# Performance work log

Measured on AMD Instinct MI355X. Metric: run time of the kernel, lower is better.

Reference implementation:

```python
import jax, jax.numpy as jnp
import numpy as np

E = 384      # EMBEDDING_SIZE
DFF = 1536
H = 6        # NUM_HEADS
D = E // H   # ATTN_DIM_SIZE = 64
T = 256      # SEQ_LEN
L = 6        # NUM_BLOCKS
V = 65       # VOCAB_SIZE
NPOS = 10000.0
B = 128


def _pos_encoding():
    i = jnp.arange(T, dtype=jnp.float32)[:, None]
    k = jnp.arange(E // 2, dtype=jnp.float32)[None, :]
    ang = i / jnp.power(NPOS, 2.0 * k / E)   # [T, E/2]
    pe = jnp.zeros((T, E), dtype=jnp.float32)
    pe = pe.at[:, 0::2].set(jnp.sin(ang))
    pe = pe.at[:, 1::2].set(jnp.cos(ang))
    return pe


def setup_inputs() -> dict:
    key = jax.random.key(0)
    ks = jax.random.split(key, 24)
    s = 0.02
    n = lambda k, shp: (jax.random.normal(k, shp, dtype=jnp.float32) * s)
    inp = {
        'tokens': jax.random.randint(ks[0], (B, T), 0, V),
        'pos_enc': _pos_encoding(),
        'emb': n(ks[1], (V, E)),
        # stacked per-layer params [L, ...]; weights stored as (in, out)
        'Wq': n(ks[2], (L, E, E)), 'bq': jnp.zeros((L, E)),
        'Wk': n(ks[3], (L, E, E)), 'bk': jnp.zeros((L, E)),
        'Wv': n(ks[4], (L, E, E)), 'bv': jnp.zeros((L, E)),
        'Wo': n(ks[5], (L, E, E)), 'bo': jnp.zeros((L, E)),
        'ln1_g': jnp.ones((L, E)), 'ln1_b': jnp.zeros((L, E)),
        'W1': n(ks[6], (L, E, DFF)), 'c1': jnp.zeros((L, DFF)),
        'W2': n(ks[7], (L, DFF, E)), 'c2': jnp.zeros((L, E)),
        'ln2_g': jnp.ones((L, E)), 'ln2_b': jnp.zeros((L, E)),
        'Wl': n(ks[8], (E, V)), 'bl': jnp.zeros((V,)),
    }
    return inp


def _layer_norm(x, g, b, eps=1e-5):
    mu = jnp.mean(x, axis=-1, keepdims=True)
    var = jnp.mean((x - mu) ** 2, axis=-1, keepdims=True)
    return (x - mu) * jax.lax.rsqrt(var + eps) * g + b


def _decoder(tokens, pos_enc, emb, Wq, bq, Wk, bk, Wv, bv, Wo, bo,
             ln1_g, ln1_b, W1, c1, W2, c2, ln2_g, ln2_b, Wl, bl):
    b_, t_ = tokens.shape
    x = emb[tokens] + pos_enc[None, :t_, :]            # [B,T,E]
    causal = jnp.tril(jnp.ones((t_, t_), dtype=bool)) # tril mask
    scale = D ** (-0.5)

    def block(x, p):
        (wq, bq_, wk, bk_, wv, bv_, wo, bo_, g1, be1, w1, c1_, w2, c2_, g2, be2) = p
        h = _layer_norm(x, g1, be1)
        q = (h @ wq + bq_).reshape(b_, t_, H, D)
        k = (h @ wk + bk_).reshape(b_, t_, H, D)
        v = (h @ wv + bv_).reshape(b_, t_, H, D)
        scores = jnp.einsum('bqhd,bkhd->bhqk', q, k) * scale
        scores = jnp.where(causal[None, None], scores, -jnp.inf)
        attn = jax.nn.softmax(scores, axis=-1)
        o = jnp.einsum('bhqk,bkhd->bqhd', attn, v).reshape(b_, t_, E)
        x = x + (o @ wo + bo_)
        h2 = _layer_norm(x, g2, be2)
        x = x + (jax.nn.relu(h2 @ w1 + c1_) @ w2 + c2_)
        return x, None

    params = (Wq, bq, Wk, bk, Wv, bv, Wo, bo, ln1_g, ln1_b, W1, c1, W2, c2, ln2_g, ln2_b)
    x, _ = jax.lax.scan(block, x, params)
    return x @ Wl + bl                                 # [B,T,V]


def reference(tokens, pos_enc, emb, Wq, bq, Wk, bk, Wv, bv, Wo, bo,
              ln1_g, ln1_b, W1, c1, W2, c2, ln2_g, ln2_b, Wl, bl):
    return _decoder(tokens, pos_enc, emb, Wq, bq, Wk, bk, Wv, bv, Wo, bo,
                    ln1_g, ln1_b, W1, c1, W2, c2, ln2_g, ln2_b, Wl, bl)
```

## Files before the change

### kernel.cpp

```cpp
#include <hip/hip_runtime.h>
#include <hip/hip_bf16.h>
#include <stdint.h>

constexpr int E   = 384;
constexpr int DFF = 1536;
constexpr int NH  = 6;
constexpr int HD  = 64;
constexpr int T   = 256;
constexpr int NL  = 6;
constexpr int NV  = 65;
constexpr int BB  = 128;
constexpr int MTOT = BB * T;
constexpr int CB  = 32;

typedef __bf16 bf16;
typedef __attribute__((ext_vector_type(8))) __bf16 bf16x8;
typedef __attribute__((ext_vector_type(4))) __bf16 bf16x4;
typedef __attribute__((ext_vector_type(4))) float floatx4;

#define GBM 128
#define GBN 128
#define GBK 64

template <int MODE, int SWAP>
__device__ __forceinline__ void gemm_body(
    char* AsB,
    const bf16* __restrict__ A, int lda,
    const bf16* __restrict__ Bf,
    const float* __restrict__ bias,
    void* __restrict__ Cv, void* __restrict__ Cv2, int ldc,
    int nt, int mt, int Nvalid, int K, int relu)
{
    int tid = threadIdx.x;
    int lane = tid & 63;
    int wid = tid >> 6;
    int wm = wid >> 2, wn = wid & 3;
    int lq = lane >> 4, lr = lane & 15;

    const bf16* Ab = A + (long)mt * GBM * lda;

    int srow = tid >> 3;
    int skc  = (tid & 7) * 8;
    const bf16* Arow = Ab + (long)srow * lda + skc;
    const long a2 = 64 * (long)lda;

    int wcol = ((tid & 7) * 16) ^ ((srow & 7) << 4);
    char* wp0 = AsB + srow * 128 + wcol;

    int nk = K / GBK;
    int nks = K / 32;
    const bf16* Bq = Bf + ((long)(nt * 8 + wn * 2) * nks) * 512 + lane * 8;

    floatx4 zero = {0.f, 0.f, 0.f, 0.f};
    floatx4 acc[4][2];
#pragma unroll
    for (int i = 0; i < 4; i++)
#pragma unroll
        for (int j = 0; j < 2; j++) acc[i][j] = zero;

    const char* rp0 = AsB + (wm * 64 + lr) * 128;
    int rx0 = (lq * 16) ^ ((lr & 7) << 4);

    bf16x8 ra[2];
    ra[0] = *(const bf16x8*)(Arow);
    ra[1] = *(const bf16x8*)(Arow + a2);
    *(bf16x8*)(wp0)        = ra[0];
    *(bf16x8*)(wp0 + 8192) = ra[1];
    if (nk > 1) {
        ra[0] = *(const bf16x8*)(Arow + GBK);
        ra[1] = *(const bf16x8*)(Arow + a2 + GBK);
    }
    __syncthreads();

    for (int ki = 0; ki < nk; ki++) {
        int ib = ki & 1;
        bf16x8 bb[4];
#pragma unroll
        for (int ni = 0; ni < 2; ni++)
#pragma unroll
            for (int kh = 0; kh < 2; kh++)
                bb[ni * 2 + kh] =
                    *(const bf16x8*)(Bq + ((long)ni * nks + 2 * ki + kh) * 512);
        if (ki + 1 < nk) {
            char* wp = wp0 + (1 - ib) * 16384;
            *(bf16x8*)(wp)        = ra[0];
            *(bf16x8*)(wp + 8192) = ra[1];
        }
        if (ki + 2 < nk) {
            long koff = (long)(ki + 2) * GBK;
            ra[0] = *(const bf16x8*)(Arow + koff);
            ra[1] = *(const bf16x8*)(Arow + a2 + koff);
        }
        const char* rp = rp0 + ib * 16384;

        bf16x8 af[4];
#pragma unroll
        for (int mi = 0; mi < 4; mi++)
            af[mi] = *(const bf16x8*)(rp + mi * 2048 + rx0);
#pragma unroll
        for (int mi = 0; mi < 4; mi++)
#pragma unroll
            for (int ni = 0; ni < 2; ni++)
                acc[mi][ni] = SWAP
                    ? __builtin_amdgcn_mfma_f32_16x16x32_bf16(bb[ni * 2], af[mi], acc[mi][ni], 0, 0, 0)
                    : __builtin_amdgcn_mfma_f32_16x16x32_bf16(af[mi], bb[ni * 2], acc[mi][ni], 0, 0, 0);
#pragma unroll
        for (int mi = 0; mi < 4; mi++)
            af[mi] = *(const bf16x8*)(rp + mi * 2048 + (rx0 ^ 64));
#pragma unroll
        for (int mi = 0; mi < 4; mi++)
#pragma unroll
            for (int ni = 0; ni < 2; ni++)
                acc[mi][ni] = SWAP
                    ? __builtin_amdgcn_mfma_f32_16x16x32_bf16(bb[ni * 2 + 1], af[mi], acc[mi][ni], 0, 0, 0)
                    : __builtin_amdgcn_mfma_f32_16x16x32_bf16(af[mi], bb[ni * 2 + 1], acc[mi][ni], 0, 0, 0);
        __syncthreads();
    }

    int m0 = mt * GBM, n0 = nt * GBN;
#pragma unroll
    for (int mi = 0; mi < 4; mi++) {
#pragma unroll
        for (int ni = 0; ni < 2; ni++) {
            floatx4 v = acc[mi][ni];
            if (SWAP) {
                int rowL = m0 + wm * 64 + mi * 16 + lr;
                int col0 = n0 + wn * 32 + ni * 16 + lq * 4;
                if (MODE == 5) {
                    bf16x4 pv;
#pragma unroll
                    for (int r = 0; r < 4; r++) pv[r] = (bf16)(v[r] + bias[col0 + r]);
                    *(bf16x4*)((bf16*)Cv + (long)rowL * 768 + col0) = pv;
                } else if (MODE == 1) {
                    bf16* Cp = (bf16*)Cv;
                    bf16x4* ptr = (bf16x4*)(Cp + (long)rowL * ldc + col0);
                    bf16x4 old = *ptr;
                    bf16x4 pv;
#pragma unroll
                    for (int r = 0; r < 4; r++)
                        pv[r] = (bf16)((float)old[r] + v[r] + bias[col0 + r]);
                    *ptr = pv;
                } else if (MODE == 4) {
                    float* Cp = (float*)Cv;
#pragma unroll
                    for (int r = 0; r < 4; r++)
                        if (col0 + r < Nvalid)
                            Cp[(long)rowL * ldc + col0 + r] = v[r] + bias[col0 + r];
                } else {
                    if (col0 < Nvalid) {
                        bf16x4 pv;
#pragma unroll
                        for (int r = 0; r < 4; r++) {
                            float x = v[r] + (bias ? bias[col0 + r] : 0.f);
                            if (relu) x = fmaxf(x, 0.f);
                            pv[r] = (bf16)x;
                        }
                        *(bf16x4*)((bf16*)Cv + (long)rowL * ldc + col0) = pv;
                    }
                }
            } else {
                int row0 = m0 + wm * 64 + mi * 16 + lq * 4;
                int colL = n0 + wn * 32 + ni * 16 + lr;
                float bv = bias[colL];
                bf16x4 pv;
#pragma unroll
                for (int r = 0; r < 4; r++) pv[r] = (bf16)(v[r] + bv);
                int bidx = row0 >> 8, pos = row0 & 255, e = colL - 768;
                *(bf16x4*)((bf16*)Cv2 + (long)bidx * (E * T) + (long)e * T + pos) = pv;
            }
        }
    }
}

template <int MODE>
__global__ __launch_bounds__(512, 4) void k_gemm(
    const bf16* __restrict__ A, int lda,
    const bf16* __restrict__ Bf,
    const float* __restrict__ bias,
    void* __restrict__ Cv, void* __restrict__ Cv2, int ldc,
    int Mtiles, int Ntiles, int Nvalid, int K,
    int relu)
{
    __shared__ __align__(16) char AsB[2 * 16384];

    int nb = gridDim.x;
    int per = nb >> 3;
    int bphys = blockIdx.x;
    int bid = (bphys & 7) * per + (bphys >> 3);

    int nt = bid % Ntiles;
    int mt = bid / Ntiles;

    if (MODE == 5 && nt >= 6)
        gemm_body<5, 0>(AsB, A, lda, Bf, bias, Cv, Cv2, ldc, nt, mt, Nvalid, K, relu);
    else
        gemm_body<MODE, 1>(AsB, A, lda, Bf, bias, Cv, Cv2, ldc, nt, mt, Nvalid, K, relu);
}

__global__ __launch_bounds__(256) void k_attn(
    const bf16* __restrict__ qk, const bf16* __restrict__ vt,
    bf16* __restrict__ o)
{
    int nb = gridDim.x;
    int per = nb >> 3;
    int bphys = blockIdx.x;
    int bid = (bphys & 7) * per + (bphys >> 3);

    int qt = bid & 3; bid >>= 2;
    int h = bid % NH; int b = bid / NH;
    int tid = threadIdx.x;
    int lane = tid & 63;
    int w = tid >> 6;
    int lq = lane >> 4;
    int lr = lane & 15;

    __shared__ __align__(16) bf16 Ks[256 * 72];
    __shared__ __align__(16) bf16 Vs[64 * 264];

    const bf16* qbase = qk + (long)(b * T + qt * 64 + w * 16) * 768 + h * 64;
    const bf16* kbase = qk + (long)(b * T) * 768 + 384 + h * 64;
    const bf16* vbase = vt + ((long)b * E + h * 64) * T;

#pragma unroll
    for (int i = 0; i < 8; i++) {
        int idx = i * 256 + tid;
        int row = idx >> 3, off = (idx & 7) * 8;
        *(bf16x8*)(&Ks[row * 72 + off]) = *(const bf16x8*)(kbase + (long)row * 768 + off);
    }
#pragma unroll
    for (int i = 0; i < 8; i++) {
        int idx = i * 256 + tid;
        int row = idx >> 5, off = (idx & 31) * 8;
        *(bf16x8*)(&Vs[row * 264 + off]) = *(const bf16x8*)(vbase + (long)row * 256 + off);
    }

    bf16x8 aq0 = *(const bf16x8*)(qbase + (long)lr * 768 + lq * 8);
    bf16x8 aq1 = *(const bf16x8*)(qbase + (long)lr * 768 + 32 + lq * 8);

    __syncthreads();

    const int ntmax = qt * 4 + 3;
    floatx4 zero = {0.f, 0.f, 0.f, 0.f};
    floatx4 s[16];
#pragma unroll
    for (int nt = 0; nt < 16; nt++) s[nt] = zero;

#pragma unroll
    for (int nt = 0; nt < 16; nt++) {
        if (nt <= ntmax) {
            const bf16* kp = &Ks[(nt * 16 + lr) * 72 + lq * 8];
            bf16x8 b0 = *(const bf16x8*)(kp);
            bf16x8 b1 = *(const bf16x8*)(kp + 32);
            s[nt] = __builtin_amdgcn_mfma_f32_16x16x32_bf16(aq0, b0, s[nt], 0, 0, 0);
            s[nt] = __builtin_amdgcn_mfma_f32_16x16x32_bf16(aq1, b1, s[nt], 0, 0, 0);
        }
    }

    int trow0 = qt * 64 + w * 16 + lq * 4;
    float m4[4] = {-3e38f, -3e38f, -3e38f, -3e38f};
#pragma unroll
    for (int nt = 0; nt < 16; nt++) {
        if (nt <= ntmax) {
            int tc = nt * 16 + lr;
#pragma unroll
            for (int r = 0; r < 4; r++) {
                float v = s[nt][r] * 0.125f;
                if (tc > trow0 + r) v = -3e38f;
                s[nt][r] = v;
                m4[r] = fmaxf(m4[r], v);
            }
        }
    }
#pragma unroll
    for (int r = 0; r < 4; r++) {
#pragma unroll
        for (int off = 1; off < 16; off <<= 1)
            m4[r] = fmaxf(m4[r], __shfl_xor(m4[r], off, 64));
    }

    float l4[4] = {0.f, 0.f, 0.f, 0.f};
#pragma unroll
    for (int nt = 0; nt < 16; nt++) {
        if (nt <= ntmax) {
#pragma unroll
            for (int r = 0; r < 4; r++) {
                float pv = __expf(s[nt][r] - m4[r]);
                l4[r] += pv;
                s[nt][r] = pv;
            }
        }
    }
#pragma unroll
    for (int r = 0; r < 4; r++) {
#pragma unroll
        for (int off = 1; off < 16; off <<= 1)
            l4[r] += __shfl_xor(l4[r], off, 64);
    }

    __syncthreads();

    bf16* P = Ks + w * (16 * 264);
#pragma unroll
    for (int nt = 0; nt < 16; nt++) {
        if (nt <= ntmax) {
#pragma unroll
            for (int r = 0; r < 4; r++)
                P[(lq * 4 + r) * 264 + nt * 16 + lr] = (bf16)s[nt][r];
        }
    }

    floatx4 oacc[4];
#pragma unroll
    for (int nd = 0; nd < 4; nd++) oacc[nd] = zero;
    const int kkmax = 2 * (qt + 1);
#pragma unroll
    for (int kk = 0; kk < 8; kk++) {
        if (kk < kkmax) {
            bf16x8 ap = *(const bf16x8*)(&P[lr * 264 + kk * 32 + lq * 8]);
#pragma unroll
            for (int nd = 0; nd < 4; nd++) {
                bf16x8 bv = *(const bf16x8*)(&Vs[(nd * 16 + lr) * 264 + kk * 32 + lq * 8]);
                oacc[nd] = __builtin_amdgcn_mfma_f32_16x16x32_bf16(ap, bv, oacc[nd], 0, 0, 0);
            }
        }
    }

#pragma unroll
    for (int r = 0; r < 4; r++) {
        float inv = 1.0f / l4[r];
        long rowg = (long)b * T + trow0 + r;
#pragma unroll
        for (int nd = 0; nd < 4; nd++) {
            o[rowg * E + h * 64 + nd * 16 + lr] = (bf16)(oacc[nd][r] * inv);
        }
    }
}

__global__ void k_ln(const bf16* __restrict__ x, const float* __restrict__ g,
                     const float* __restrict__ b, bf16* __restrict__ h) {
    int row = blockIdx.x * 4 + (threadIdx.x >> 6);
    int lane = threadIdx.x & 63;
    const bf16* xr = x + (long)row * E;
    float v[6];
    float s = 0.f;
#pragma unroll
    for (int i = 0; i < 6; i++) { v[i] = (float)xr[lane + 64 * i]; s += v[i]; }
#pragma unroll
    for (int o = 1; o < 64; o <<= 1) s += __shfl_xor(s, o, 64);
    float mu = s * (1.0f / E);
    float q = 0.f;
#pragma unroll
    for (int i = 0; i < 6; i++) { float d = v[i] - mu; q += d * d; }
#pragma unroll
    for (int o = 1; o < 64; o <<= 1) q += __shfl_xor(q, o, 64);
    float rs = rsqrtf(q * (1.0f / E) + 1e-5f);
    bf16* hr = h + (long)row * E;
#pragma unroll
    for (int i = 0; i < 6; i++) {
        int c = lane + 64 * i;
        hr[c] = (bf16)((v[i] - mu) * rs * g[c] + b[c]);
    }
}

__global__ void k_transpose_frag(const float* __restrict__ W, bf16* __restrict__ Wf,
                                 int K, int N, int NPAD) {
    long idx = (long)blockIdx.x * 256 + threadIdx.x;
    long per = (long)NPAD * K;
    int l = (int)(idx / per);
    long r = idx - (long)l * per;
    int j = (int)(r & 7); r >>= 3;
    int lane = (int)(r & 63); r >>= 6;
    int nks = K / 32;
    int ks = (int)(r % nks);
    int c16 = (int)(r / nks);
    int col = c16 * 16 + (lane & 15);
    int k = ks * 32 + (lane >> 4) * 8 + j;
    Wf[idx] = (col < N) ? (bf16)W[((long)l * K + k) * N + col] : (bf16)0.0f;
}

__global__ void k_transpose_qkv_frag(const float* __restrict__ Wq, const float* __restrict__ Wk,
                                     const float* __restrict__ Wv, bf16* __restrict__ Wf) {
    long idx = (long)blockIdx.x * 256 + threadIdx.x;
    long per = (long)1152 * E;
    int l = (int)(idx / per);
    long r = idx - (long)l * per;
    int j = (int)(r & 7); r >>= 3;
    int lane = (int)(r & 63); r >>= 6;
    int nks = E / 32;
    int ks = (int)(r % nks);
    int c16 = (int)(r / nks);
    int col = c16 * 16 + (lane & 15);
    int k = ks * 32 + (lane >> 4) * 8 + j;
    const float* src;
    int cc;
    if (col < 384)      { src = Wq; cc = col; }
    else if (col < 768) { src = Wk; cc = col - 384; }
    else                { src = Wv; cc = col - 768; }
    Wf[idx] = (bf16)src[((long)l * E + k) * E + cc];
}

__global__ void k_bias_qkv(const float* __restrict__ bq, const float* __restrict__ bk,
                           const float* __restrict__ bv, float* __restrict__ bqkv) {
    int idx = blockIdx.x * 256 + threadIdx.x;
    int l = idx / 1152;
    int j = idx - l * 1152;
    const float* src;
    int jj;
    if (j < 384)      { src = bq; jj = j; }
    else if (j < 768) { src = bk; jj = j - 384; }
    else              { src = bv; jj = j - 768; }
    bqkv[idx] = src[l * E + jj];
}

__global__ void k_embed(const int* __restrict__ tokens, const float* __restrict__ pos,
                        const float* __restrict__ emb, bf16* __restrict__ x) {
    long idx = (long)blockIdx.x * 256 + threadIdx.x;
    int e = (int)(idx % E);
    long bt = idx / E;
    int t = (int)(bt % T);
    int tok = tokens[bt];
    x[idx] = (bf16)(emb[(long)tok * E + e] + pos[(long)t * E + e]);
}

extern "C" void kernel_launch(void* const* d_in, const int* in_sizes, int n_in,
                              void* d_out, int out_size, void* d_ws, size_t ws_size,
                              hipStream_t stream) {
    const int*   tokens = (const int*)d_in[0];
    const float* pos  = (const float*)d_in[1];
    const float* emb  = (const float*)d_in[2];
    const float* Wq   = (const float*)d_in[3];
    const float* bq   = (const float*)d_in[4];
    const float* Wk   = (const float*)d_in[5];
    const float* bk   = (const float*)d_in[6];
    const float* Wv   = (const float*)d_in[7];
    const float* bv   = (const float*)d_in[8];
    const float* Wo   = (const float*)d_in[9];
    const float* bo   = (const float*)d_in[10];
    const float* g1   = (const float*)d_in[11];
    const float* be1  = (const float*)d_in[12];
    const float* W1   = (const float*)d_in[13];
    const float* c1   = (const float*)d_in[14];
    const float* W2   = (const float*)d_in[15];
    const float* c2   = (const float*)d_in[16];
    const float* g2   = (const float*)d_in[17];
    const float* be2  = (const float*)d_in[18];
    const float* Wl   = (const float*)d_in[19];
    const float* bl   = (const float*)d_in[20];

    char* p = (char*)d_ws;
    bf16* x  = (bf16*)p;   p += (long)MTOT * E * 2;
    bf16* h  = (bf16*)p;   p += (long)MTOT * E * 2;
    bf16* qk = (bf16*)p;   p += (long)MTOT * 768 * 2;
    bf16* vt = (bf16*)p;   p += (long)BB * E * T * 2;
    bf16* SP = (bf16*)p;   p += (long)CB * NH * T * T * 2;
    bf16* WqkvF = (bf16*)p; p += (long)NL * 1152 * E * 2;
    bf16* WoF = (bf16*)p;  p += (long)NL * E * E * 2;
    bf16* W1F = (bf16*)p;  p += (long)NL * DFF * E * 2;
    bf16* W2F = (bf16*)p;  p += (long)NL * E * DFF * 2;
    bf16* WlF = (bf16*)p;  p += (long)128 * E * 2;
    float* bqkv = (float*)p; p += (long)NL * 1152 * 4;
    bf16* mid = qk;
    bf16* o   = h;
    (void)SP;

    k_transpose_qkv_frag<<<(NL * 1152 * E) / 256, 256, 0, stream>>>(Wq, Wk, Wv, WqkvF);
    k_transpose_frag<<<(NL * E * E) / 256, 256, 0, stream>>>(Wo, WoF, E, E, E);
    k_transpose_frag<<<(NL * DFF * E) / 256, 256, 0, stream>>>(W1, W1F, E, DFF, DFF);
    k_transpose_frag<<<(NL * E * DFF) / 256, 256, 0, stream>>>(W2, W2F, DFF, E, E);
    k_transpose_frag<<<(128 * E) / 256, 256, 0, stream>>>(Wl, WlF, E, NV, 128);
    k_bias_qkv<<<(NL * 1152) / 256, 256, 0, stream>>>(bq, bk, bv, bqkv);

    k_embed<<<(MTOT * E) / 256, 256, 0, stream>>>(tokens, pos, emb, x);

    for (int l = 0; l < NL; l++) {
        k_ln<<<MTOT / 4, 256, 0, stream>>>(x, g1 + l * E, be1 + l * E, h);
        k_gemm<5><<<256 * 9, 512, 0, stream>>>(h, E, WqkvF + (long)l * 1152 * E,
                                               bqkv + l * 1152, qk, vt, 0,
                                               256, 9, 1152, E, 0);
        k_attn<<<BB * NH * 4, 256, 0, stream>>>(qk, vt, o);
        k_gemm<1><<<256 * 3, 512, 0, stream>>>(o, E, WoF + (long)l * E * E,
                                               bo + l * E, x, nullptr, E,
                                               256, 3, E, E, 0);
        k_ln<<<MTOT / 4, 256, 0, stream>>>(x, g2 + l * E, be2 + l * E, h);
        k_gemm<0><<<256 * 12, 512, 0, stream>>>(h, E, W1F + (long)l * DFF * E,
                                                c1 + l * DFF, mid, nullptr, DFF,
                                                256, 12, DFF, E, 1);
        k_gemm<1><<<256 * 3, 512, 0, stream>>>(mid, DFF, W2F + (long)l * E * DFF,
                                               c2 + l * E, x, nullptr, E,
                                               256, 3, E, DFF, 0);
    }

    k_gemm<4><<<256 * 1, 512, 0, stream>>>(x, E, WlF,
                                           bl, d_out, nullptr, NV,
                                           256, 1, NV, E, 0);
}
```

Before: 1.774 ms.

## Load GEMM A tiles directly into LDS via global_load_lds with pre-swizzled addresses

Swaps the register-staged A-tile path (global load into registers, then LDS store) for direct global-to-LDS loads with 16-byte width. The XOR swizzle moves from the LDS write address to the global source column, so each lane's contiguous LDS slot matches the old swizzled layout. The prefetch distance drops from two stages to one. Launch bounds also rise to 6 waves per SIMD to press for higher occupancy. This saves VGPRs and VALU/LDS store instructions, at the cost of less latency hiding and possible register spills under the tighter launch bound.

```diff
diff --git a/kernel.cpp b/kernel.cpp
--- a/kernel.cpp
+++ b/kernel.cpp
@@ -17,6 +17,12 @@
 typedef __attribute__((ext_vector_type(8))) __bf16 bf16x8;
 typedef __attribute__((ext_vector_type(4))) __bf16 bf16x4;
 typedef __attribute__((ext_vector_type(4))) float floatx4;
+
+__device__ __forceinline__ void gload_lds16(const void* g, void* l) {
+    __builtin_amdgcn_global_load_lds(
+        (const __attribute__((address_space(1))) void*)g,
+        (__attribute__((address_space(3))) void*)l, 16, 0, 0);
+}
 
 #define GBM 128
 #define GBN 128
@@ -40,12 +46,11 @@
     const bf16* Ab = A + (long)mt * GBM * lda;
 
     int srow = tid >> 3;
-    int skc  = (tid & 7) * 8;
+    int slot = tid & 7;
+    int skc  = (slot ^ (srow & 7)) * 8;
     const bf16* Arow = Ab + (long)srow * lda + skc;
     const long a2 = 64 * (long)lda;
-
-    int wcol = ((tid & 7) * 16) ^ ((srow & 7) << 4);
-    char* wp0 = AsB + srow * 128 + wcol;
+    int wofs = wid * 1024;
 
     int nk = K / GBK;
     int nks = K / 32;
@@ -61,15 +66,12 @@
     const char* rp0 = AsB + (wm * 64 + lr) * 128;
     int rx0 = (lq * 16) ^ ((lr & 7) << 4);
 
-    bf16x8 ra[2];
-    ra[0] = *(const bf16x8*)(Arow);
-    ra[1] = *(const bf16x8*)(Arow + a2);
-    *(bf16x8*)(wp0)        = ra[0];
-    *(bf16x8*)(wp0 + 8192) = ra[1];
-    if (nk > 1) {
-        ra[0] = *(const bf16x8*)(Arow + GBK);
-        ra[1] = *(const bf16x8*)(Arow + a2 + GBK);
-    }
+    {
+        char* base = AsB + wofs;
+        gload_lds16(Arow,      base);
+        gload_lds16(Arow + a2, base + 8192);
+    }
+    asm volatile("s_waitcnt vmcnt(0)" ::: "memory");
     __syncthreads();
 
     for (int ki = 0; ki < nk; ki++) {
@@ -82,14 +84,10 @@
                 bb[ni * 2 + kh] =
                     *(const bf16x8*)(Bq + ((long)ni * nks + 2 * ki + kh) * 512);
         if (ki + 1 < nk) {
-            char* wp = wp0 + (1 - ib) * 16384;
-            *(bf16x8*)(wp)        = ra[0];
-            *(bf16x8*)(wp + 8192) = ra[1];
-        }
-        if (ki + 2 < nk) {
-            long koff = (long)(ki + 2) * GBK;
-            ra[0] = *(const bf16x8*)(Arow + koff);
-            ra[1] = *(const bf16x8*)(Arow + a2 + koff);
+            long koff = (long)(ki + 1) * GBK;
+            char* base = AsB + (1 - ib) * 16384 + wofs;
+            gload_lds16(Arow + koff,      base);
+            gload_lds16(Arow + a2 + koff, base + 8192);
         }
         const char* rp = rp0 + ib * 16384;
 
@@ -173,7 +171,7 @@
 }
 
 template <int MODE>
-__global__ __launch_bounds__(512, 4) void k_gemm(
+__global__ __launch_bounds__(512, 6) void k_gemm(
     const bf16* __restrict__ A, int lda,
     const bf16* __restrict__ Bf,
     const float* __restrict__ bias,
```

After: 1.676 ms. 1.06x faster.
